# Performance work log

Measured on AMD Instinct MI355X. Metric: run time of the kernel, lower is better.

## Reference

```python
import jax, jax.numpy as jnp
import numpy as np

N = 100000
E = 800000
D = 128
THETA = (0.5, 0.3, 0.2)
NEG_SLOPE = 0.01  # torch F.leaky_relu default


def setup_inputs() -> dict:
    key = jax.random.key(0)
    ks = jax.random.split(key, 16)
    inv = 1.0 / np.sqrt(D)
    return {
        "src": jax.random.randint(ks[0], (E,), 0, N),
        "dst": jax.random.randint(ks[1], (E,), 0, N),
        "x0": jax.random.normal(ks[2], (N, D), jnp.float32),
        "x": jax.random.normal(ks[3], (N, D), jnp.float32),
        "e": jax.random.normal(ks[4], (N, D), jnp.float32),
        "labels": jax.random.randint(ks[5], (N,), 0, 2),
        "nid": jax.random.randint(ks[6], (N // 2,), 0, N),
        "alpha": jnp.full((1,), 0.5, jnp.float32),
        "emb": jax.random.normal(ks[7], (3, D), jnp.float32).at[2].set(0.0),  # padding_idx=2
        "pred_w1": jax.random.normal(ks[8], (D, D), jnp.float32) * inv,
        "pred_b1": jnp.zeros((D,), jnp.float32),
        "pred_w2": jax.random.normal(ks[9], (2, D), jnp.float32) * inv,
        "pred_b2": jnp.zeros((2,), jnp.float32),
        "weights": jax.random.uniform(ks[10], (2 * D, D), jnp.float32, -inv, inv),
        "lin_w": jax.random.normal(ks[11], (D, 2 * D), jnp.float32) * inv,
        "lin_b": jnp.zeros((D,), jnp.float32),
    }


def reference(src, dst, x0, x, e, labels, nid, alpha, emb,
              pred_w1, pred_b1, pred_w2, pred_b2, weights, lin_w, lin_b):
    # Predictor: MLP -> 2 logits, prob of class 1
    h = jax.nn.relu(x @ pred_w1.T + pred_b1)
    logits = h @ pred_w2.T + pred_b2                     # [N, 2]
    prob = jax.nn.softmax(logits, axis=1)[:, 1]          # [N]

    # NodeLabelEmbedding: soft mix of rows 0 and 1
    x_node = (1.0 - prob)[:, None] * emb[0] + prob[:, None] * emb[1]
    x_ = x
    xk = x + alpha * x_node

    # degree norm from edge list (in-degrees at dst)
    degs = jax.ops.segment_sum(jnp.ones_like(dst, dtype=xk.dtype), dst, num_segments=N)
    dinv = jnp.clip(degs, 1.0, None) ** -0.5             # [N]
    dinv = dinv[:, None]

    def unn_laplacian(feat):
        # feat - D^-1/2 A D^-1/2 feat  (messages src -> dst)
        msg = jax.ops.segment_sum((feat * dinv)[src], dst, num_segments=N)
        return feat - msg * dinv

    hi = THETA[0] * xk
    for k in range(1, len(THETA)):
        xk = unn_laplacian(xk)
        hi = hi + THETA[k] * xk

    hi = jnp.concatenate([hi, x_], axis=1)               # [N, 2D]
    outputs = hi @ weights                               # [N, D]
    out = jnp.concatenate([e, outputs], axis=1)          # [N, 2D]
    out = jax.nn.leaky_relu(out @ lin_w.T + lin_b, NEG_SLOPE)
    return out + x0                                      # residual
```

## Files before the change

### kernel.cpp

```cpp
#include <hip/hip_runtime.h>

#define N_NODES 100000
#define N_EDGES 800000
#define D 128

typedef __attribute__((ext_vector_type(8))) short short8;
typedef __attribute__((ext_vector_type(4))) float f32x4;

__device__ inline unsigned short f2bf(float f) {
  unsigned u = __float_as_uint(f);
  unsigned r = (u + 0x7fffu + ((u >> 16) & 1u)) >> 16;
  return (unsigned short)r;
}
__device__ inline void bfma8(float* acc, const uint4 v, float d) {
  acc[0] = fmaf(__uint_as_float(v.x << 16), d, acc[0]);
  acc[1] = fmaf(__uint_as_float(v.x & 0xffff0000u), d, acc[1]);
  acc[2] = fmaf(__uint_as_float(v.y << 16), d, acc[2]);
  acc[3] = fmaf(__uint_as_float(v.y & 0xffff0000u), d, acc[3]);
  acc[4] = fmaf(__uint_as_float(v.z << 16), d, acc[4]);
  acc[5] = fmaf(__uint_as_float(v.z & 0xffff0000u), d, acc[5]);
  acc[6] = fmaf(__uint_as_float(v.w << 16), d, acc[6]);
  acc[7] = fmaf(__uint_as_float(v.w & 0xffff0000u), d, acc[7]);
}
__device__ inline void unpack8(float* o, const uint4 v) {
  o[0] = __uint_as_float(v.x << 16); o[1] = __uint_as_float(v.x & 0xffff0000u);
  o[2] = __uint_as_float(v.y << 16); o[3] = __uint_as_float(v.y & 0xffff0000u);
  o[4] = __uint_as_float(v.z << 16); o[5] = __uint_as_float(v.z & 0xffff0000u);
  o[6] = __uint_as_float(v.w << 16); o[7] = __uint_as_float(v.w & 0xffff0000u);
}
__device__ inline uint4 pack8(const float* v) {
  uint4 r;
  r.x = (unsigned)f2bf(v[0]) | ((unsigned)f2bf(v[1]) << 16);
  r.y = (unsigned)f2bf(v[2]) | ((unsigned)f2bf(v[3]) << 16);
  r.z = (unsigned)f2bf(v[4]) | ((unsigned)f2bf(v[5]) << 16);
  r.w = (unsigned)f2bf(v[6]) | ((unsigned)f2bf(v[7]) << 16);
  return r;
}

__global__ void k_deg(const int* __restrict__ dst, int* __restrict__ degs) {
  int e = blockIdx.x * 256 + threadIdx.x;
  if (e < N_EDGES) atomicAdd(&degs[dst[e]], 1);
}

__global__ void k_scan1(const int* __restrict__ degs, int* __restrict__ offs,
                        int* __restrict__ aux) {
  __shared__ int s[256];
  int tid = threadIdx.x;
  int i = blockIdx.x * 256 + tid;
  int v = (i < N_NODES) ? degs[i] : 0;
  int sum = v;
  s[tid] = sum; __syncthreads();
  for (int off = 1; off < 256; off <<= 1) {
    int t = (tid >= off) ? s[tid - off] : 0;
    __syncthreads();
    sum += t; s[tid] = sum;
    __syncthreads();
  }
  if (i < N_NODES) offs[i] = sum - v;
  if (tid == 255) aux[blockIdx.x] = sum;
}

__global__ void k_scan2(const int* __restrict__ aux, int* __restrict__ aux2, int nblk) {
  __shared__ int s[512];
  int tid = threadIdx.x;
  int v = (tid < nblk) ? aux[tid] : 0;
  int sum = v;
  s[tid] = sum; __syncthreads();
  for (int off = 1; off < 512; off <<= 1) {
    int t = (tid >= off) ? s[tid - off] : 0;
    __syncthreads();
    sum += t; s[tid] = sum;
    __syncthreads();
  }
  aux2[tid] = sum - v;
}

__global__ void k_scan3(int* __restrict__ offs, const int* __restrict__ aux2,
                        const int* __restrict__ degs, float* __restrict__ dinv) {
  int i = blockIdx.x * 256 + threadIdx.x;
  if (i < N_NODES) {
    offs[i] += aux2[blockIdx.x];
    dinv[i] = rsqrtf(fmaxf((float)degs[i], 1.0f));
  }
}

__global__ void k_fill(const int* __restrict__ src, const int* __restrict__ dst,
                       const int* __restrict__ offs, int* __restrict__ cursor,
                       int* __restrict__ csr) {
  int e = blockIdx.x * 256 + threadIdx.x;
  if (e < N_EDGES) {
    int d = dst[e];
    int pos = offs[d] + atomicAdd(&cursor[d], 1);
    csr[pos] = src[e];
  }
}

__global__ __launch_bounds__(256, 2)
void k_mlp(const float* __restrict__ x, const float* __restrict__ w1,
           const float* __restrict__ w2, const float* __restrict__ b1,
           const float* __restrict__ b2, const float* __restrict__ emb,
           const float* __restrict__ alpha_p, unsigned short* __restrict__ xk_bf) {
  __shared__ __align__(16) float xsT[128 * 68];
  __shared__ __align__(16) float w1sT[32 * 128];
  __shared__ float zbuf[64];
  __shared__ float pbuf[64];

  int tid = threadIdx.x;
  int lane = tid & 63;
  int wave = tid >> 6;
  int n0 = blockIdx.x * 64;

  {
    int n = lane;
    int gn = n0 + n;
    const float4* xr = (const float4*)(x + (size_t)gn * 128 + wave * 32);
    #pragma unroll
    for (int i = 0; i < 8; i++) {
      float4 v = make_float4(0.f, 0.f, 0.f, 0.f);
      if (gn < N_NODES) v = xr[i];
      int k = wave * 32 + i * 4;
      xsT[(k + 0) * 68 + n] = v.x;
      xsT[(k + 1) * 68 + n] = v.y;
      xsT[(k + 2) * 68 + n] = v.z;
      xsT[(k + 3) * 68 + n] = v.w;
    }
  }

  int d8 = tid & 15;
  int n4 = tid >> 4;
  float acc[4][8];
  #pragma unroll
  for (int a = 0; a < 4; a++)
    #pragma unroll
    for (int c = 0; c < 8; c++) acc[a][c] = 0.f;

  for (int p = 0; p < 4; p++) {
    __syncthreads();
    {
      int j = tid >> 1;
      int kg0 = (tid & 1) * 4;
      const float4* wr = (const float4*)(w1 + j * 128 + p * 32);
      #pragma unroll
      for (int c = 0; c < 4; c++) {
        float4 v = wr[kg0 + c];
        int k = (kg0 + c) * 4;
        w1sT[(k + 0) * 128 + j] = v.x;
        w1sT[(k + 1) * 128 + j] = v.y;
        w1sT[(k + 2) * 128 + j] = v.z;
        w1sT[(k + 3) * 128 + j] = v.w;
      }
    }
    __syncthreads();

    for (int kk = 0; kk < 32; kk += 4) {
      float wq[4][8];
      float4 f[4];
      #pragma unroll
      for (int q = 0; q < 4; q++) {
        const float4* wr = (const float4*)(w1sT + (kk + q) * 128 + d8 * 8);
        float4 a = wr[0], b = wr[1];
        wq[q][0] = a.x; wq[q][1] = a.y; wq[q][2] = a.z; wq[q][3] = a.w;
        wq[q][4] = b.x; wq[q][5] = b.y; wq[q][6] = b.z; wq[q][7] = b.w;
        f[q] = *(const float4*)(xsT + (p * 32 + kk + q) * 68 + n4 * 4);
      }
      #pragma unroll
      for (int q = 0; q < 4; q++) {
        #pragma unroll
        for (int c = 0; c < 8; c++) {
          acc[0][c] += f[q].x * wq[q][c];
          acc[1][c] += f[q].y * wq[q][c];
          acc[2][c] += f[q].z * wq[q][c];
          acc[3][c] += f[q].w * wq[q][c];
        }
      }
    }
  }

  {
    int j0 = d8 * 8;
    float bb[8], wd[8];
    #pragma unroll
    for (int c = 0; c < 8; c++) {
      bb[c] = b1[j0 + c];
      wd[c] = w2[128 + j0 + c] - w2[j0 + c];
    }
    #pragma unroll
    for (int a = 0; a < 4; a++) {
      float s = 0.f;
      #pragma unroll
      for (int c = 0; c < 8; c++) {
        float h = fmaxf(acc[a][c] + bb[c], 0.f);
        s += h * wd[c];
      }
      s += __shfl_down(s, 8);
      s += __shfl_down(s, 4);
      s += __shfl_down(s, 2);
      s += __shfl_down(s, 1);
      if (d8 == 0) zbuf[n4 * 4 + a] = s;
    }
  }
  __syncthreads();
  if (tid < 64) {
    float db2 = b2[1] - b2[0];
    float z = zbuf[tid] + db2;
    pbuf[tid] = 1.f / (1.f + expf(-z));
  }
  __syncthreads();

  {
    float al = alpha_p[0];
    int d4 = tid & 31;
    const float4 e0 = ((const float4*)emb)[d4];
    const float4 e1 = ((const float4*)(emb + 128))[d4];
    #pragma unroll
    for (int i = 0; i < 8; i++) {
      int n = i * 8 + (tid >> 5);
      int gn = n0 + n;
      if (gn >= N_NODES) continue;
      float p = pbuf[n];
      float c0 = al * (1.f - p), c1 = al * p;
      float4 xv = ((const float4*)x)[(size_t)gn * 32 + d4];
      float o0 = xv.x + c0 * e0.x + c1 * e1.x;
      float o1 = xv.y + c0 * e0.y + c1 * e1.y;
      float o2 = xv.z + c0 * e0.z + c1 * e1.z;
      float o3 = xv.w + c0 * e0.w + c1 * e1.w;
      ushort4 ov = make_ushort4(f2bf(o0), f2bf(o1), f2bf(o2), f2bf(o3));
      ((ushort4*)xk_bf)[(size_t)gn * 32 + d4] = ov;
    }
  }
}

template <int PASS>
__global__ __launch_bounds__(256)
void k_gather(const unsigned short* __restrict__ feat,
              unsigned short* __restrict__ feat_out,
              float* __restrict__ hi,
              unsigned short* __restrict__ ahi,
              const int* __restrict__ csr, const int* __restrict__ offs,
              const int* __restrict__ degs, const float* __restrict__ dinv) {
  int node = blockIdx.x * 4 + (threadIdx.x >> 6);
  int lane = threadIdx.x & 63;
  int quad = lane >> 4;
  int l16 = lane & 15;
  int start = offs[node];
  int cnt = degs[node];
  const uint4* f16 = (const uint4*)feat;
  float acc[8];
  #pragma unroll
  for (int i = 0; i < 8; i++) acc[i] = 0.f;

  int j = 0;
  for (; j + 8 <= cnt; j += 8) {
    int sa = csr[start + j + quad];
    int sb = csr[start + j + 4 + quad];
    float da = dinv[sa], db = dinv[sb];
    uint4 va = f16[(size_t)sa * 16 + l16];
    uint4 vb = f16[(size_t)sb * 16 + l16];
    bfma8(acc, va, da);
    bfma8(acc, vb, db);
  }
  if (j + 4 <= cnt) {
    int s = csr[start + j + quad];
    float d = dinv[s];
    uint4 v = f16[(size_t)s * 16 + l16];
    bfma8(acc, v, d);
    j += 4;
  }
  int rem = cnt - j;
  if (quad < rem) {
    int s = csr[start + j + quad];
    float d = dinv[s];
    uint4 v = f16[(size_t)s * 16 + l16];
    bfma8(acc, v, d);
  }

  #pragma unroll
  for (int i = 0; i < 8; i++) {
    acc[i] += __shfl_down(acc[i], 32);
    acc[i] += __shfl_down(acc[i], 16);
  }

  if (quad == 0) {
    float dvi = dinv[node];
    float old[8], nw[8];
    unpack8(old, f16[(size_t)node * 16 + l16]);
    #pragma unroll
    for (int i = 0; i < 8; i++) nw[i] = old[i] - acc[i] * dvi;
    if (PASS == 1) {
      ((uint4*)feat_out)[(size_t)node * 16 + l16] = pack8(nw);
      float h[8];
      #pragma unroll
      for (int i = 0; i < 8; i++) h[i] = 0.5f * old[i] + 0.3f * nw[i];
      float4* hp = (float4*)(hi + (size_t)node * 128 + l16 * 8);
      hp[0] = make_float4(h[0], h[1], h[2], h[3]);
      hp[1] = make_float4(h[4], h[5], h[6], h[7]);
    } else {
      const float4* hp = (const float4*)(hi + (size_t)node * 128 + l16 * 8);
      float4 a = hp[0], b = hp[1];
      float h[8] = {a.x, a.y, a.z, a.w, b.x, b.y, b.z, b.w};
      #pragma unroll
      for (int i = 0; i < 8; i++) h[i] += 0.2f * nw[i];
      ((uint4*)ahi)[(size_t)node * 16 + l16] = pack8(h);
    }
  }
}

__global__ void k_pre(const float* __restrict__ weights, const float* __restrict__ lin_w,
                      unsigned short* __restrict__ wbt) {
  int gid = blockIdx.x * 256 + threadIdx.x;
  int k = gid >> 7, d = gid & 127;
  float v;
  if (k < 128) {
    v = lin_w[d * 256 + k];
  } else {
    const float* wrow = weights + (k - 128) * 128;
    const float* lcol = lin_w + d * 256 + 128;
    float s = 0.f;
    for (int j = 0; j < 128; j++) s += wrow[j] * lcol[j];
    v = s;
  }
  wbt[d * 392 + k] = f2bf(v);
}

__global__ __launch_bounds__(256, 2)
void k_gemm2(const float* __restrict__ ein, const unsigned short* __restrict__ ahi,
             const float* __restrict__ x, const unsigned short* __restrict__ wbt,
             const float* __restrict__ lin_b, const float* __restrict__ x0,
             float* __restrict__ out) {
  __shared__ __align__(16) unsigned short Bs[64 * 392];
  int tid = threadIdx.x;
  int lane = tid & 63, wv = tid >> 6;
  int quad = lane >> 4, l16 = lane & 15;
  int n0 = blockIdx.x * 64;
  int rA = n0 + wv * 16 + l16;
  if (rA >= N_NODES) rA = N_NODES - 1;
  int kq = quad * 8;

  short8 af[12];
  #pragma unroll
  for (int kb = 0; kb < 4; kb++) {
    const float4* p = (const float4*)(ein + (size_t)rA * 128 + kb * 32 + kq);
    float4 a = p[0], b = p[1];
    short8 t;
    t[0] = (short)f2bf(a.x); t[1] = (short)f2bf(a.y);
    t[2] = (short)f2bf(a.z); t[3] = (short)f2bf(a.w);
    t[4] = (short)f2bf(b.x); t[5] = (short)f2bf(b.y);
    t[6] = (short)f2bf(b.z); t[7] = (short)f2bf(b.w);
    af[kb] = t;
  }
  #pragma unroll
  for (int kb = 0; kb < 4; kb++)
    af[4 + kb] = *(const short8*)(ahi + (size_t)rA * 128 + kb * 32 + kq);
  #pragma unroll
  for (int kb = 0; kb < 4; kb++) {
    const float4* p = (const float4*)(x + (size_t)rA * 128 + kb * 32 + kq);
    float4 a = p[0], b = p[1];
    short8 t;
    t[0] = (short)f2bf(a.x); t[1] = (short)f2bf(a.y);
    t[2] = (short)f2bf(a.z); t[3] = (short)f2bf(a.w);
    t[4] = (short)f2bf(b.x); t[5] = (short)f2bf(b.y);
    t[6] = (short)f2bf(b.z); t[7] = (short)f2bf(b.w);
    af[8 + kb] = t;
  }

  f32x4 acc[8];
  #pragma unroll
  for (int i = 0; i < 8; i++) acc[i] = (f32x4){0.f, 0.f, 0.f, 0.f};

  for (int h = 0; h < 2; h++) {
    if (h) __syncthreads();
    {
      const uint4* W = (const uint4*)wbt;
      uint4* B4 = (uint4*)Bs;
      int r = tid >> 2, c0 = tid & 3;
      #pragma unroll
      for (int i = 0; i < 13; i++) {
        int c = c0 + i * 4;
        if (c < 49) B4[r * 49 + c] = W[(h * 64 + r) * 49 + c];
      }
    }
    __syncthreads();
    #pragma unroll
    for (int kb = 0; kb < 12; kb++) {
      short8 a = af[kb];
      #pragma unroll
      for (int t = 0; t < 4; t++) {
        short8 b = *(const short8*)(Bs + (t * 16 + l16) * 392 + kb * 32 + kq);
        acc[h * 4 + t] = __builtin_amdgcn_mfma_f32_16x16x32_bf16(a, b, acc[h * 4 + t], 0, 0, 0);
      }
    }
  }

  #pragma unroll
  for (int idx = 0; idx < 8; idx++) {
    int col = (idx >> 2) * 64 + (idx & 3) * 16 + l16;
    float bl = lin_b[col];
    #pragma unroll
    for (int r = 0; r < 4; r++) {
      int gn = n0 + wv * 16 + quad * 4 + r;
      if (gn < N_NODES) {
        float v = acc[idx][r] + bl;
        v = (v > 0.f) ? v : 0.01f * v;
        out[(size_t)gn * 128 + col] = v + x0[(size_t)gn * 128 + col];
      }
    }
  }
}

extern "C" void kernel_launch(void* const* d_in, const int* in_sizes, int n_in,
                              void* d_out, int out_size, void* d_ws, size_t ws_size,
                              hipStream_t stream) {
  const int*   src     = (const int*)d_in[0];
  const int*   dst     = (const int*)d_in[1];
  const float* x0      = (const float*)d_in[2];
  const float* x       = (const float*)d_in[3];
  const float* ein     = (const float*)d_in[4];
  const float* alpha   = (const float*)d_in[7];
  const float* emb     = (const float*)d_in[8];
  const float* w1      = (const float*)d_in[9];
  const float* b1      = (const float*)d_in[10];
  const float* w2      = (const float*)d_in[11];
  const float* b2      = (const float*)d_in[12];
  const float* weights = (const float*)d_in[13];
  const float* lin_w   = (const float*)d_in[14];
  const float* lin_b   = (const float*)d_in[15];
  float* out = (float*)d_out;

  unsigned short* xk_bf  = (unsigned short*)d_ws;
  unsigned short* xk1_bf = xk_bf  + (size_t)N_NODES * 128;
  unsigned short* ahi    = xk1_bf + (size_t)N_NODES * 128;
  unsigned short* wbt    = ahi    + (size_t)N_NODES * 128;
  float* dinv = (float*)(wbt + 128 * 392);
  int* degs   = (int*)(dinv + N_NODES);
  int* offs   = degs + N_NODES;
  int* cursor = offs + N_NODES;
  int* aux    = cursor + N_NODES;
  int* aux2   = aux + 512;
  int* csr    = aux2 + 512;

  hipMemsetAsync(degs, 0, sizeof(int) * 3 * (size_t)N_NODES, stream);

  int gE = (N_EDGES + 255) / 256;
  int gN = (N_NODES + 255) / 256;
  k_deg  <<<gE, 256, 0, stream>>>(dst, degs);
  k_scan1<<<gN, 256, 0, stream>>>(degs, offs, aux);
  k_scan2<<<1, 512, 0, stream>>>(aux, aux2, gN);
  k_scan3<<<gN, 256, 0, stream>>>(offs, aux2, degs, dinv);
  k_fill <<<gE, 256, 0, stream>>>(src, dst, offs, cursor, csr);

  k_mlp<<<(N_NODES + 63) / 64, 256, 0, stream>>>(x, w1, w2, b1, b2, emb, alpha, xk_bf);
  k_pre<<<192, 256, 0, stream>>>(weights, lin_w, wbt);

  float* hi = out;
  k_gather<1><<<N_NODES / 4, 256, 0, stream>>>(xk_bf,  xk1_bf, hi, nullptr, csr, offs, degs, dinv);
  k_gather<2><<<N_NODES / 4, 256, 0, stream>>>(xk1_bf, nullptr, hi, ahi,    csr, offs, degs, dinv);

  k_gemm2<<<(N_NODES + 63) / 64, 256, 0, stream>>>(ein, ahi, x, wbt, lin_b, x0, out);
}
```

Before: 492.8 us.

## Pre-swizzle GEMM weights into MFMA fragment order and read directly from global

```diff
diff --git a/kernel.cpp b/kernel.cpp
--- a/kernel.cpp
+++ b/kernel.cpp
@@ -306,7 +306,7 @@
 }
 
 __global__ void k_pre(const float* __restrict__ weights, const float* __restrict__ lin_w,
-                      unsigned short* __restrict__ wbt) {
+                      unsigned short* __restrict__ wbtf) {
   int gid = blockIdx.x * 256 + threadIdx.x;
   int k = gid >> 7, d = gid & 127;
   float v;
@@ -319,15 +319,18 @@
     for (int j = 0; j < 128; j++) s += wrow[j] * lcol[j];
     v = s;
   }
-  wbt[d * 392 + k] = f2bf(v);
-}
-
-__global__ __launch_bounds__(256, 2)
+  int kb = k >> 5, kr = k & 31;
+  int quad = kr >> 3, j = kr & 7;
+  int t = d >> 4, l16 = d & 15;
+  int lane = quad * 16 + l16;
+  wbtf[(((kb * 8 + t) * 64 + lane) << 3) + j] = f2bf(v);
+}
+
+__global__ __launch_bounds__(256, 4)
 void k_gemm2(const float* __restrict__ ein, const unsigned short* __restrict__ ahi,
-             const float* __restrict__ x, const unsigned short* __restrict__ wbt,
+             const float* __restrict__ x, const unsigned short* __restrict__ wbtf,
              const float* __restrict__ lin_b, const float* __restrict__ x0,
              float* __restrict__ out) {
-  __shared__ __align__(16) unsigned short Bs[64 * 392];
   int tid = threadIdx.x;
   int lane = tid & 63, wv = tid >> 6;
   int quad = lane >> 4, l16 = lane & 15;
@@ -367,39 +370,26 @@
   #pragma unroll
   for (int i = 0; i < 8; i++) acc[i] = (f32x4){0.f, 0.f, 0.f, 0.f};
 
-  for (int h = 0; h < 2; h++) {
-    if (h) __syncthreads();
-    {
-      const uint4* W = (const uint4*)wbt;
-      uint4* B4 = (uint4*)Bs;
-      int r = tid >> 2, c0 = tid & 3;
-      #pragma unroll
-      for (int i = 0; i < 13; i++) {
-        int c = c0 + i * 4;
-        if (c < 49) B4[r * 49 + c] = W[(h * 64 + r) * 49 + c];
-      }
-    }
-    __syncthreads();
-    #pragma unroll
-    for (int kb = 0; kb < 12; kb++) {
-      short8 a = af[kb];
-      #pragma unroll
-      for (int t = 0; t < 4; t++) {
-        short8 b = *(const short8*)(Bs + (t * 16 + l16) * 392 + kb * 32 + kq);
-        acc[h * 4 + t] = __builtin_amdgcn_mfma_f32_16x16x32_bf16(a, b, acc[h * 4 + t], 0, 0, 0);
-      }
-    }
-  }
-
-  #pragma unroll
-  for (int idx = 0; idx < 8; idx++) {
-    int col = (idx >> 2) * 64 + (idx & 3) * 16 + l16;
+  const short8* bf = (const short8*)wbtf;
+  #pragma unroll
+  for (int kb = 0; kb < 12; kb++) {
+    short8 a = af[kb];
+    #pragma unroll
+    for (int t = 0; t < 8; t++) {
+      short8 b = bf[(kb * 8 + t) * 64 + lane];
+      acc[t] = __builtin_amdgcn_mfma_f32_16x16x32_bf16(a, b, acc[t], 0, 0, 0);
+    }
+  }
+
+  #pragma unroll
+  for (int t = 0; t < 8; t++) {
+    int col = t * 16 + l16;
     float bl = lin_b[col];
     #pragma unroll
     for (int r = 0; r < 4; r++) {
       int gn = n0 + wv * 16 + quad * 4 + r;
       if (gn < N_NODES) {
-        float v = acc[idx][r] + bl;
+        float v = acc[t][r] + bl;
         v = (v > 0.f) ? v : 0.01f * v;
         out[(size_t)gn * 128 + col] = v + x0[(size_t)gn * 128 + col];
       }
@@ -429,8 +419,8 @@
   unsigned short* xk_bf  = (unsigned short*)d_ws;
   unsigned short* xk1_bf = xk_bf  + (size_t)N_NODES * 128;
   unsigned short* ahi    = xk1_bf + (size_t)N_NODES * 128;
-  unsigned short* wbt    = ahi    + (size_t)N_NODES * 128;
-  float* dinv = (float*)(wbt + 128 * 392);
+  unsigned short* wbtf   = ahi    + (size_t)N_NODES * 128;
+  float* dinv = (float*)(wbtf + 12 * 8 * 64 * 8);
   int* degs   = (int*)(dinv + N_NODES);
   int* offs   = degs + N_NODES;
   int* cursor = offs + N_NODES;
@@ -449,11 +439,11 @@
   k_fill <<<gE, 256, 0, stream>>>(src, dst, offs, cursor, csr);
 
   k_mlp<<<(N_NODES + 63) / 64, 256, 0, stream>>>(x, w1, w2, b1, b2, emb, alpha, xk_bf);
-  k_pre<<<192, 256, 0, stream>>>(weights, lin_w, wbt);
+  k_pre<<<192, 256, 0, stream>>>(weights, lin_w, wbtf);
 
   float* hi = out;
   k_gather<1><<<N_NODES / 4, 256, 0, stream>>>(xk_bf,  xk1_bf, hi, nullptr, csr, offs, degs, dinv);
   k_gather<2><<<N_NODES / 4, 256, 0, stream>>>(xk1_bf, nullptr, hi, ahi,    csr, offs, degs, dinv);
 
-  k_gemm2<<<(N_NODES + 63) / 64, 256, 0, stream>>>(ein, ahi, x, wbt, lin_b, x0, out);
-}
+  k_gemm2<<<(N_NODES + 63) / 64, 256, 0, stream>>>(ein, ahi, x, wbtf, lin_b, x0, out);
+}
```

Measured after the change: 504.8 us. 1.02x slower.
